# Performance work log

Hardware: AMD Instinct MI355X
Metric: run time of the kernel (lower is better)

Reference implementation:

```python
import jax, jax.numpy as jnp
import numpy as np

B, F, H, D, S = 32, 512, 8, 64, 256
TOPK = max(1, int(0.1 * F))  # 51
BETA0 = 0.6


def setup_inputs() -> dict:
    key = jax.random.key(0)
    k1, k2, k3 = jax.random.split(key, 3)
    values = jax.random.normal(k1, (B, F, H, D), jnp.float32)
    data_logits = jax.random.normal(k2, (B, F, H, S), jnp.float32)
    # alpha is orthogonal-initialized in torch; normal init preserves the math being tested
    alpha = jax.random.normal(k3, (H, S, F), jnp.float32)
    inv_softplus = np.float32(BETA0 + np.log1p(-np.exp(-BETA0)))
    beta_param = jnp.full((H, S, 1), inv_softplus, jnp.float32)
    return {"values": values, "data_logits": data_logits, "alpha": alpha, "beta_param": beta_param}


def _topk_mask(logits, k):
    # keep exactly top-k per row (last axis), others -> -inf (matches torch topk+scatter)
    topv, topi = jax.lax.top_k(logits, k)            # [..., k]
    shp = logits.shape
    n = int(np.prod(shp[:-1]))
    flat = jnp.full((n, shp[-1]), -jnp.inf, logits.dtype)
    rows = jnp.arange(n)[:, None]
    flat = flat.at[rows, topi.reshape(n, k)].set(topv.reshape(n, k))
    return flat.reshape(shp)


def reference(values, data_logits, alpha, beta_param):
    scale = 1.0 / np.sqrt(alpha.shape[-1])
    alpha_logits = alpha * scale                       # [H,S,F]
    dl = jnp.transpose(data_logits, (0, 2, 3, 1))      # [B,H,S,F]
    mu = dl.mean(axis=-1, keepdims=True)
    std = jnp.sqrt(dl.var(axis=-1, keepdims=True) + 1e-6) + 1e-6
    dl = (dl - mu) / std
    beta_eff = jax.nn.softplus(beta_param)             # [H,S,1]
    logits = alpha_logits[None] + beta_eff[None] * dl  # [B,H,S,F]
    logits = _topk_mask(logits, TOPK)
    attn = jax.nn.softmax(logits, axis=-1)             # dropout omitted (eval mode)
    out = jnp.einsum('bhsf,bfhd->bshd', attn, values)  # [B,S,H,D]
    return out
```

## Files before the change

kernel.cpp:

```cpp
#include <hip/hip_runtime.h>
#include <hip/hip_bf16.h>
#include <stdint.h>
#include <math.h>

#define NB 32
#define NF 512
#define NH 8
#define ND 64
#define NS 256
#define TOPK 51
#define STILE 16
#define LDSF 537

__device__ __forceinline__ float wave_sum_f32(float v) {
#pragma unroll
  for (int o = 32; o > 0; o >>= 1) v += __shfl_xor(v, o, 64);
  return v;
}

__device__ __forceinline__ int lane_prefix(unsigned long long m) {
  return __builtin_amdgcn_mbcnt_hi((unsigned)(m >> 32),
         __builtin_amdgcn_mbcnt_lo((unsigned)m, 0u));
}

__device__ __forceinline__ unsigned f32key(float x) {
  unsigned b = __float_as_uint(x);
  return (b & 0x80000000u) ? ~b : (b | 0x80000000u);
}

__device__ __forceinline__ float np_pairwise_sum_512(const float* __restrict__ row, int lane) {
  const int c2 = lane & 31;
  const int k  = c2 >> 3;
  const int c  = c2 & 7;
  const float* blk = row + 136 * k;
  float r = blk[c];
#pragma unroll
  for (int m = 1; m < 16; ++m) r += blk[c + 8 * m];
  float s = r + __shfl_xor(r, 1, 64);
  s = s + __shfl_xor(s, 2, 64);
  s = s + __shfl_xor(s, 4, 64);
  float u = s + __shfl_xor(s, 8, 64);
  u = u + __shfl_xor(u, 16, 64);
  return u;
}

__global__ __launch_bounds__(256)
void prep_kernel(const float* __restrict__ bp, const float* __restrict__ alpha,
                 float* __restrict__ betaf, unsigned* __restrict__ klo,
                 unsigned* __restrict__ khi) {
  const int gid  = blockIdx.x * 256 + threadIdx.x;
  const int hs   = gid >> 6;
  const int lane = gid & 63;
  if (hs >= NH * NS) return;
  const float scalef = (float)0.04419417382415922;
  const float* ar = alpha + (size_t)hs * NF;
  float s1 = 0.f, s2 = 0.f;
#pragma unroll
  for (int j = 0; j < 8; ++j) {
    float v = ar[lane + 64 * j] * scalef;
    s1 += v; s2 = fmaf(v, v, s2);
  }
  s1 = wave_sum_f32(s1); s2 = wave_sum_f32(s2);
  const float mean = s1 * (1.f / 512.f);
  float var = s2 * (1.f / 512.f) - mean * mean;
  if (var < 0.f) var = 0.f;
  const double e = exp((double)bp[hs]);
  const float beta = (float)log1p(e);
  const float sig  = sqrtf(var + beta * beta);
  const float that = fmaf(1.281552f, sig, mean);
  const float w    = 0.30f * sig;
  if (lane == 0) {
    betaf[hs] = beta;
    klo[hs] = f32key(that - w);
    khi[hs] = f32key(that + w);
  }
}

__global__ __launch_bounds__(1024, 8)
void gating_attention_kernel(const float* __restrict__ vals,
                             const float* __restrict__ dlg,
                             const float* __restrict__ alpha,
                             const float* __restrict__ betap,
                             const float* __restrict__ betaf,
                             const unsigned* __restrict__ klo,
                             const unsigned* __restrict__ khi,
                             float* __restrict__ out)
{
#pragma clang fp contract(off)
  __shared__ float dl_t[STILE * LDSF];
  __shared__ uint2 pairs[STILE][64];

  const int blk  = blockIdx.x;
  const int bh   = blk & 255;
  const int t    = blk >> 8;
  const int b    = bh >> 3;
  const int h    = bh & 7;
  const int s0   = t * STILE;
  const int tid  = threadIdx.x;
  const int w    = tid >> 6;
  const int lane = tid & 63;
  const float scalef = (float)0.04419417382415922;

#pragma unroll
  for (int cc = 0; cc < 2; ++cc) {
    int i  = cc * 1024 + tid;
    int f  = i >> 2;
    int sg = (i & 3) << 2;
    int fo = f + ((f >> 7) << 3);
    const float4 v4 = *reinterpret_cast<const float4*>(
        dlg + ((((size_t)b * NF + f) * NH + h) * NS + (size_t)(s0 + sg)));
    dl_t[(sg + 0) * LDSF + fo] = v4.x;
    dl_t[(sg + 1) * LDSF + fo] = v4.y;
    dl_t[(sg + 2) * LDSF + fo] = v4.z;
    dl_t[(sg + 3) * LDSF + fo] = v4.w;
  }
  __syncthreads();

  const int s  = s0 + w;
  const int hs = h * NS + s;
  float* row = dl_t + w * LDSF;

  const int fb0 = 4 * lane;
  const int off0 = fb0 + ((fb0 >> 7) << 3);
  const int fb1 = 256 + 4 * lane;
  const int off1 = fb1 + ((fb1 >> 7) << 3);

  const float4 a40 = *reinterpret_cast<const float4*>(
      alpha + ((size_t)hs) * NF + fb0);
  const float4 a41 = *reinterpret_cast<const float4*>(
      alpha + ((size_t)hs) * NF + fb1);
  const float4 x40 = *reinterpret_cast<const float4*>(row + off0);
  const float4 x41 = *reinterpret_cast<const float4*>(row + off1);

  float a[8] = {a40.x, a40.y, a40.z, a40.w, a41.x, a41.y, a41.z, a41.w};
  float x[8] = {x40.x, x40.y, x40.z, x40.w, x41.x, x41.y, x41.z, x41.w};

  const float S1 = np_pairwise_sum_512(row, lane);
  const float mu = S1 * (1.0f / 512.0f);

  float tv[8];
#pragma unroll
  for (int j = 0; j < 8; ++j) tv[j] = x[j] - mu;
  *reinterpret_cast<float4*>(row + off0) =
      make_float4(tv[0]*tv[0], tv[1]*tv[1], tv[2]*tv[2], tv[3]*tv[3]);
  *reinterpret_cast<float4*>(row + off1) =
      make_float4(tv[4]*tv[4], tv[5]*tv[5], tv[6]*tv[6], tv[7]*tv[7]);
  const float S2  = np_pairwise_sum_512(row, lane);
  const float var = S2 * (1.0f / 512.0f);
  const float stdv = sqrtf(var + 1e-6f) + 1e-6f;

  float beta;
  if (betaf) beta = betaf[hs];
  else { double e = exp((double)betap[hs]); beta = (float)log1p(e); }

  const double rd = 1.0 / (double)stdv;
  float lg[8];
  unsigned key[8];
#pragma unroll
  for (int j = 0; j < 8; ++j) {
    float z  = (float)((double)tv[j] * rd);
    float m  = beta * z;
    float af = a[j] * scalef;
    float l  = af + m;
    lg[j] = l;
    key[j] = f32key(l);
  }

  auto countGE = [&key](unsigned thr) -> int {
    int c = 0;
#pragma unroll
    for (int j = 0; j < 8; ++j) c += __popcll(__ballot(key[j] >= thr));
    return c;
  };

  unsigned lo, hi;
  if (klo) {
    lo = klo[hs]; hi = khi[hs];
    if (hi <= lo) hi = lo + 1;
  } else {
    unsigned kmax = key[0], kmin = key[0];
#pragma unroll
    for (int j = 1; j < 8; ++j) {
      kmax = key[j] > kmax ? key[j] : kmax;
      kmin = key[j] < kmin ? key[j] : kmin;
    }
#pragma unroll
    for (int o = 32; o > 0; o >>= 1) {
      unsigned om = (unsigned)__shfl_xor((int)kmax, o, 64);
      unsigned on = (unsigned)__shfl_xor((int)kmin, o, 64);
      kmax = om > kmax ? om : kmax;
      kmin = on < kmin ? on : kmin;
    }
    lo = kmin; hi = kmax;
  }

  int cl = countGE(lo);
  unsigned step = hi - lo;
  while (cl < TOPK) {
    hi = lo;
    lo = (lo >= step) ? (lo - step) : 0u;
    step <<= 1;
    cl = countGE(lo);
  }
  unsigned T; int cnt;
  if (cl == TOPK) { T = lo; cnt = cl; }
  else {
    int ch = countGE(hi);
    while (ch >= TOPK && hi != 0xFFFFFFFFu) {
      lo = hi; cl = ch;
      unsigned nh = hi + step;
      if (nh < hi) nh = 0xFFFFFFFFu;
      hi = nh; step <<= 1;
      ch = countGE(hi);
    }
    if (ch >= TOPK) { T = hi; cnt = ch; }
    else {
      while (lo < hi) {
        unsigned mid = hi - ((hi - lo) >> 1);
        int cm = countGE(mid);
        if (cm >= TOPK) { lo = mid; cl = cm; if (cm == TOPK) break; }
        else hi = mid - 1;
      }
      T = lo; cnt = cl;
    }
  }
  const bool exact = (cnt == TOPK);

  bool keep[8];
  if (exact) {
#pragma unroll
    for (int j = 0; j < 8; ++j) keep[j] = (key[j] >= T);
  } else {
    int g = 0;
#pragma unroll
    for (int j = 0; j < 8; ++j) g += __popcll(__ballot(key[j] > T));
    const int need = TOPK - g;
    int cumt = 0;
#pragma unroll
    for (int j = 0; j < 8; ++j) {
      unsigned long long meq = __ballot(key[j] == T);
      int tr = cumt + lane_prefix(meq);
      cumt += __popcll(meq);
      keep[j] = (key[j] > T) || ((key[j] == T) && (tr < need));
    }
  }

  unsigned tb = (T & 0x80000000u) ? (T ^ 0x80000000u) : ~T;
  const float thrf = __uint_as_float(tb);

  float p[8];
  float zs = 0.0f;
#pragma unroll
  for (int j = 0; j < 8; ++j) {
    float e = keep[j] ? __expf(lg[j] - thrf) : 0.0f;
    p[j] = e;
    zs += e;
  }
  zs = wave_sum_f32(zs);
  const float rz = 1.0f / zs;

  int base = 0;
#pragma unroll
  for (int j = 0; j < 8; ++j) {
    unsigned long long mk = __ballot(keep[j]);
    int idx = base + lane_prefix(mk);
    if (keep[j]) {
      unsigned f = (unsigned)(((j >> 2) << 8) + 4 * lane + (j & 3));
      pairs[w][idx] = make_uint2(f << 11, __float_as_uint(p[j]));
    }
    base += __popcll(mk);
  }
  if (lane == TOPK) pairs[w][TOPK] = make_uint2(0u, 0u);
  const int nk = (TOPK + 3) & ~3;

  const char* vbase = (const char*)(vals + (((size_t)b * NF) * NH + h) * ND) + 4 * lane;
  float acc0 = 0.0f, acc1 = 0.0f, acc2 = 0.0f, acc3 = 0.0f;
  for (int k0 = 0; k0 < nk; k0 += 4) {
    uint2 e0 = pairs[w][k0 + 0];
    uint2 e1 = pairs[w][k0 + 1];
    uint2 e2 = pairs[w][k0 + 2];
    uint2 e3 = pairs[w][k0 + 3];
    float v0 = *(const float*)(vbase + e0.x);
    float v1 = *(const float*)(vbase + e1.x);
    float v2 = *(const float*)(vbase + e2.x);
    float v3 = *(const float*)(vbase + e3.x);
    acc0 = fmaf(__uint_as_float(e0.y), v0, acc0);
    acc1 = fmaf(__uint_as_float(e1.y), v1, acc1);
    acc2 = fmaf(__uint_as_float(e2.y), v2, acc2);
    acc3 = fmaf(__uint_as_float(e3.y), v3, acc3);
  }
  const float acc = (acc0 + acc1) + (acc2 + acc3);

  out[(((size_t)b * NS + s) * NH + h) * ND + lane] = acc * rz;
}

extern "C" void kernel_launch(void* const* d_in, const int* in_sizes, int n_in,
                              void* d_out, int out_size, void* d_ws, size_t ws_size,
                              hipStream_t stream) {
  const float* vals  = (const float*)d_in[0];
  const float* dlg   = (const float*)d_in[1];
  const float* alpha = (const float*)d_in[2];
  const float* betap = (const float*)d_in[3];
  float* out = (float*)d_out;

  float* betaf = nullptr; unsigned* klo = nullptr; unsigned* khi = nullptr;
  const size_t need = (size_t)(NH * NS) * 12;
  if (ws_size >= need) {
    betaf = (float*)d_ws;
    klo   = (unsigned*)((char*)d_ws + (size_t)(NH * NS) * 4);
    khi   = (unsigned*)((char*)d_ws + (size_t)(NH * NS) * 8);
    prep_kernel<<<(NH * NS * 64) / 256, 256, 0, stream>>>(betap, alpha, betaf, klo, khi);
  }

  dim3 grid(NB * NH * (NS / STILE));
  dim3 block(1024);
  gating_attention_kernel<<<grid, block, 0, stream>>>(vals, dlg, alpha, betap,
                                                      betaf, klo, khi, out);
}
```

Before: 106.8 us.

## Process two sequence rows per wave with a 32-row tile and reuse LDS for pairs

New measurement: 132.3 us. 23.9% more time.

```diff
diff --git a/kernel.cpp b/kernel.cpp
--- a/kernel.cpp
+++ b/kernel.cpp
@@ -9,7 +9,7 @@
 #define ND 64
 #define NS 256
 #define TOPK 51
-#define STILE 16
+#define STILE 32
 #define LDSF 537
 
 __device__ __forceinline__ float wave_sum_f32(float v) {
@@ -42,6 +42,42 @@
   float u = s + __shfl_xor(s, 8, 64);
   u = u + __shfl_xor(u, 16, 64);
   return u;
+}
+
+__device__ __forceinline__ void solve_topk(const unsigned key[8], unsigned lo, unsigned hi,
+                                           unsigned& T, int& cnt) {
+  auto countGE = [&key](unsigned thr) -> int {
+    int c = 0;
+#pragma unroll
+    for (int j = 0; j < 8; ++j) c += __popcll(__ballot(key[j] >= thr));
+    return c;
+  };
+  if (hi <= lo) hi = lo + 1;
+  int cl = countGE(lo);
+  unsigned step = hi - lo;
+  while (cl < TOPK) {
+    hi = lo;
+    lo = (lo >= step) ? (lo - step) : 0u;
+    step <<= 1;
+    cl = countGE(lo);
+  }
+  if (cl == TOPK) { T = lo; cnt = cl; return; }
+  int ch = countGE(hi);
+  while (ch >= TOPK && hi != 0xFFFFFFFFu) {
+    lo = hi; cl = ch;
+    unsigned nh = hi + step;
+    if (nh < hi) nh = 0xFFFFFFFFu;
+    hi = nh; step <<= 1;
+    ch = countGE(hi);
+  }
+  if (ch >= TOPK) { T = hi; cnt = ch; return; }
+  while (lo < hi) {
+    unsigned mid = hi - ((hi - lo) >> 1);
+    int cm = countGE(mid);
+    if (cm >= TOPK) { lo = mid; cl = cm; if (cm == TOPK) break; }
+    else hi = mid - 1;
+  }
+  T = lo; cnt = cl;
 }
 
 __global__ __launch_bounds__(256)
@@ -88,7 +124,6 @@
 {
 #pragma clang fp contract(off)
   __shared__ float dl_t[STILE * LDSF];
-  __shared__ uint2 pairs[STILE][64];
 
   const int blk  = blockIdx.x;
   const int bh   = blk & 255;
@@ -102,10 +137,10 @@
   const float scalef = (float)0.04419417382415922;
 
 #pragma unroll
-  for (int cc = 0; cc < 2; ++cc) {
+  for (int cc = 0; cc < 4; ++cc) {
     int i  = cc * 1024 + tid;
-    int f  = i >> 2;
-    int sg = (i & 3) << 2;
+    int f  = i >> 3;
+    int sg = (i & 7) << 2;
     int fo = f + ((f >> 7) << 3);
     const float4 v4 = *reinterpret_cast<const float4*>(
         dlg + ((((size_t)b * NF + f) * NH + h) * NS + (size_t)(s0 + sg)));
@@ -116,73 +151,88 @@
   }
   __syncthreads();
 
-  const int s  = s0 + w;
-  const int hs = h * NS + s;
-  float* row = dl_t + w * LDSF;
+  const int r0 = 2 * w, r1 = 2 * w + 1;
+  const int sA = s0 + r0, sB = s0 + r1;
+  const int hsA = h * NS + sA, hsB = h * NS + sB;
+  float* rowA = dl_t + r0 * LDSF;
+  float* rowB = dl_t + r1 * LDSF;
 
   const int fb0 = 4 * lane;
   const int off0 = fb0 + ((fb0 >> 7) << 3);
   const int fb1 = 256 + 4 * lane;
   const int off1 = fb1 + ((fb1 >> 7) << 3);
 
-  const float4 a40 = *reinterpret_cast<const float4*>(
-      alpha + ((size_t)hs) * NF + fb0);
-  const float4 a41 = *reinterpret_cast<const float4*>(
-      alpha + ((size_t)hs) * NF + fb1);
-  const float4 x40 = *reinterpret_cast<const float4*>(row + off0);
-  const float4 x41 = *reinterpret_cast<const float4*>(row + off1);
-
-  float a[8] = {a40.x, a40.y, a40.z, a40.w, a41.x, a41.y, a41.z, a41.w};
-  float x[8] = {x40.x, x40.y, x40.z, x40.w, x41.x, x41.y, x41.z, x41.w};
-
-  const float S1 = np_pairwise_sum_512(row, lane);
-  const float mu = S1 * (1.0f / 512.0f);
-
-  float tv[8];
-#pragma unroll
-  for (int j = 0; j < 8; ++j) tv[j] = x[j] - mu;
-  *reinterpret_cast<float4*>(row + off0) =
-      make_float4(tv[0]*tv[0], tv[1]*tv[1], tv[2]*tv[2], tv[3]*tv[3]);
-  *reinterpret_cast<float4*>(row + off1) =
-      make_float4(tv[4]*tv[4], tv[5]*tv[5], tv[6]*tv[6], tv[7]*tv[7]);
-  const float S2  = np_pairwise_sum_512(row, lane);
-  const float var = S2 * (1.0f / 512.0f);
-  const float stdv = sqrtf(var + 1e-6f) + 1e-6f;
-
-  float beta;
-  if (betaf) beta = betaf[hs];
-  else { double e = exp((double)betap[hs]); beta = (float)log1p(e); }
-
-  const double rd = 1.0 / (double)stdv;
-  float lg[8];
-  unsigned key[8];
+  const float4 aA0 = *reinterpret_cast<const float4*>(alpha + (size_t)hsA * NF + fb0);
+  const float4 aA1 = *reinterpret_cast<const float4*>(alpha + (size_t)hsA * NF + fb1);
+  const float4 aB0 = *reinterpret_cast<const float4*>(alpha + (size_t)hsB * NF + fb0);
+  const float4 aB1 = *reinterpret_cast<const float4*>(alpha + (size_t)hsB * NF + fb1);
+  const float4 xA0 = *reinterpret_cast<const float4*>(rowA + off0);
+  const float4 xA1 = *reinterpret_cast<const float4*>(rowA + off1);
+  const float4 xB0 = *reinterpret_cast<const float4*>(rowB + off0);
+  const float4 xB1 = *reinterpret_cast<const float4*>(rowB + off1);
+
+  float xA[8] = {xA0.x, xA0.y, xA0.z, xA0.w, xA1.x, xA1.y, xA1.z, xA1.w};
+  float xB[8] = {xB0.x, xB0.y, xB0.z, xB0.w, xB1.x, xB1.y, xB1.z, xB1.w};
+  float aA[8] = {aA0.x, aA0.y, aA0.z, aA0.w, aA1.x, aA1.y, aA1.z, aA1.w};
+  float aB[8] = {aB0.x, aB0.y, aB0.z, aB0.w, aB1.x, aB1.y, aB1.z, aB1.w};
+
+  const float S1A = np_pairwise_sum_512(rowA, lane);
+  const float S1B = np_pairwise_sum_512(rowB, lane);
+  const float muA = S1A * (1.0f / 512.0f);
+  const float muB = S1B * (1.0f / 512.0f);
+
+  float tvA[8], tvB[8];
+#pragma unroll
+  for (int j = 0; j < 8; ++j) { tvA[j] = xA[j] - muA; tvB[j] = xB[j] - muB; }
+  *reinterpret_cast<float4*>(rowA + off0) =
+      make_float4(tvA[0]*tvA[0], tvA[1]*tvA[1], tvA[2]*tvA[2], tvA[3]*tvA[3]);
+  *reinterpret_cast<float4*>(rowA + off1) =
+      make_float4(tvA[4]*tvA[4], tvA[5]*tvA[5], tvA[6]*tvA[6], tvA[7]*tvA[7]);
+  *reinterpret_cast<float4*>(rowB + off0) =
+      make_float4(tvB[0]*tvB[0], tvB[1]*tvB[1], tvB[2]*tvB[2], tvB[3]*tvB[3]);
+  *reinterpret_cast<float4*>(rowB + off1) =
+      make_float4(tvB[4]*tvB[4], tvB[5]*tvB[5], tvB[6]*tvB[6], tvB[7]*tvB[7]);
+  const float S2A = np_pairwise_sum_512(rowA, lane);
+  const float S2B = np_pairwise_sum_512(rowB, lane);
+  const float stdA = sqrtf(S2A * (1.0f / 512.0f) + 1e-6f) + 1e-6f;
+  const float stdB = sqrtf(S2B * (1.0f / 512.0f) + 1e-6f) + 1e-6f;
+
+  float betaA, betaB;
+  if (betaf) { betaA = betaf[hsA]; betaB = betaf[hsB]; }
+  else {
+    betaA = (float)log1p(exp((double)betap[hsA]));
+    betaB = (float)log1p(exp((double)betap[hsB]));
+  }
+
+  const double rdA = 1.0 / (double)stdA;
+  const double rdB = 1.0 / (double)stdB;
+  float lgA[8], lgB[8];
+  unsigned keyA[8], keyB[8];
 #pragma unroll
   for (int j = 0; j < 8; ++j) {
-    float z  = (float)((double)tv[j] * rd);
-    float m  = beta * z;
-    float af = a[j] * scalef;
-    float l  = af + m;
-    lg[j] = l;
-    key[j] = f32key(l);
-  }
-
-  auto countGE = [&key](unsigned thr) -> int {
-    int c = 0;
-#pragma unroll
-    for (int j = 0; j < 8; ++j) c += __popcll(__ballot(key[j] >= thr));
-    return c;
-  };
-
-  unsigned lo, hi;
+    float zA = (float)((double)tvA[j] * rdA);
+    float zB = (float)((double)tvB[j] * rdB);
+    float lA = aA[j] * scalef + betaA * zA;
+    float lB = aB[j] * scalef + betaB * zB;
+    lgA[j] = lA; lgB[j] = lB;
+    keyA[j] = f32key(lA); keyB[j] = f32key(lB);
+  }
+
+  unsigned loA, hiA, loB, hiB;
   if (klo) {
-    lo = klo[hs]; hi = khi[hs];
-    if (hi <= lo) hi = lo + 1;
+    loA = klo[hsA]; hiA = khi[hsA];
+    loB = klo[hsB]; hiB = khi[hsB];
   } else {
-    unsigned kmax = key[0], kmin = key[0];
+    unsigned kmin = keyA[0], kmax = keyA[0];
 #pragma unroll
     for (int j = 1; j < 8; ++j) {
-      kmax = key[j] > kmax ? key[j] : kmax;
-      kmin = key[j] < kmin ? key[j] : kmin;
+      kmax = keyA[j] > kmax ? keyA[j] : kmax;
+      kmin = keyA[j] < kmin ? keyA[j] : kmin;
+    }
+#pragma unroll
+    for (int j = 0; j < 8; ++j) {
+      kmax = keyB[j] > kmax ? keyB[j] : kmax;
+      kmin = keyB[j] < kmin ? keyB[j] : kmin;
     }
 #pragma unroll
     for (int o = 32; o > 0; o >>= 1) {
@@ -191,107 +241,116 @@
       kmax = om > kmax ? om : kmax;
       kmin = on < kmin ? on : kmin;
     }
-    lo = kmin; hi = kmax;
-  }
-
-  int cl = countGE(lo);
-  unsigned step = hi - lo;
-  while (cl < TOPK) {
-    hi = lo;
-    lo = (lo >= step) ? (lo - step) : 0u;
-    step <<= 1;
-    cl = countGE(lo);
-  }
-  unsigned T; int cnt;
-  if (cl == TOPK) { T = lo; cnt = cl; }
-  else {
-    int ch = countGE(hi);
-    while (ch >= TOPK && hi != 0xFFFFFFFFu) {
-      lo = hi; cl = ch;
-      unsigned nh = hi + step;
-      if (nh < hi) nh = 0xFFFFFFFFu;
-      hi = nh; step <<= 1;
-      ch = countGE(hi);
-    }
-    if (ch >= TOPK) { T = hi; cnt = ch; }
-    else {
-      while (lo < hi) {
-        unsigned mid = hi - ((hi - lo) >> 1);
-        int cm = countGE(mid);
-        if (cm >= TOPK) { lo = mid; cl = cm; if (cm == TOPK) break; }
-        else hi = mid - 1;
-      }
-      T = lo; cnt = cl;
-    }
-  }
-  const bool exact = (cnt == TOPK);
-
-  bool keep[8];
-  if (exact) {
-#pragma unroll
-    for (int j = 0; j < 8; ++j) keep[j] = (key[j] >= T);
+    loA = loB = kmin; hiA = hiB = kmax;
+  }
+  unsigned TA, TB; int cntA, cntB;
+  solve_topk(keyA, loA, hiA, TA, cntA);
+  solve_topk(keyB, loB, hiB, TB, cntB);
+
+  bool keepA[8], keepB[8];
+  if (cntA == TOPK) {
+#pragma unroll
+    for (int j = 0; j < 8; ++j) keepA[j] = (keyA[j] >= TA);
   } else {
     int g = 0;
 #pragma unroll
-    for (int j = 0; j < 8; ++j) g += __popcll(__ballot(key[j] > T));
+    for (int j = 0; j < 8; ++j) g += __popcll(__ballot(keyA[j] > TA));
     const int need = TOPK - g;
     int cumt = 0;
 #pragma unroll
     for (int j = 0; j < 8; ++j) {
-      unsigned long long meq = __ballot(key[j] == T);
+      unsigned long long meq = __ballot(keyA[j] == TA);
       int tr = cumt + lane_prefix(meq);
       cumt += __popcll(meq);
-      keep[j] = (key[j] > T) || ((key[j] == T) && (tr < need));
-    }
-  }
-
-  unsigned tb = (T & 0x80000000u) ? (T ^ 0x80000000u) : ~T;
-  const float thrf = __uint_as_float(tb);
-
-  float p[8];
-  float zs = 0.0f;
+      keepA[j] = (keyA[j] > TA) || ((keyA[j] == TA) && (tr < need));
+    }
+  }
+  if (cntB == TOPK) {
+#pragma unroll
+    for (int j = 0; j < 8; ++j) keepB[j] = (keyB[j] >= TB);
+  } else {
+    int g = 0;
+#pragma unroll
+    for (int j = 0; j < 8; ++j) g += __popcll(__ballot(keyB[j] > TB));
+    const int need = TOPK - g;
+    int cumt = 0;
+#pragma unroll
+    for (int j = 0; j < 8; ++j) {
+      unsigned long long meq = __ballot(keyB[j] == TB);
+      int tr = cumt + lane_prefix(meq);
+      cumt += __popcll(meq);
+      keepB[j] = (keyB[j] > TB) || ((keyB[j] == TB) && (tr < need));
+    }
+  }
+
+  unsigned tbA = (TA & 0x80000000u) ? (TA ^ 0x80000000u) : ~TA;
+  unsigned tbB = (TB & 0x80000000u) ? (TB ^ 0x80000000u) : ~TB;
+  const float thrA = __uint_as_float(tbA);
+  const float thrB = __uint_as_float(tbB);
+
+  float pA[8], pB[8];
+  float zsA = 0.0f, zsB = 0.0f;
 #pragma unroll
   for (int j = 0; j < 8; ++j) {
-    float e = keep[j] ? __expf(lg[j] - thrf) : 0.0f;
-    p[j] = e;
-    zs += e;
-  }
-  zs = wave_sum_f32(zs);
-  const float rz = 1.0f / zs;
-
-  int base = 0;
+    float eA = keepA[j] ? __expf(lgA[j] - thrA) : 0.0f;
+    float eB = keepB[j] ? __expf(lgB[j] - thrB) : 0.0f;
+    pA[j] = eA; pB[j] = eB;
+    zsA += eA; zsB += eB;
+  }
+  zsA = wave_sum_f32(zsA);
+  zsB = wave_sum_f32(zsB);
+  const float rzA = 1.0f / zsA;
+  const float rzB = 1.0f / zsB;
+
+  uint2* prA = (uint2*)(dl_t + ((r0 * LDSF + 1) & ~1));
+  uint2* prB = (uint2*)(dl_t + ((r1 * LDSF + 1) & ~1));
+  int baseA = 0, baseB = 0;
 #pragma unroll
   for (int j = 0; j < 8; ++j) {
-    unsigned long long mk = __ballot(keep[j]);
-    int idx = base + lane_prefix(mk);
-    if (keep[j]) {
-      unsigned f = (unsigned)(((j >> 2) << 8) + 4 * lane + (j & 3));
-      pairs[w][idx] = make_uint2(f << 11, __float_as_uint(p[j]));
-    }
-    base += __popcll(mk);
-  }
-  if (lane == TOPK) pairs[w][TOPK] = make_uint2(0u, 0u);
+    unsigned f = (unsigned)(((j >> 2) << 8) + 4 * lane + (j & 3));
+    unsigned long long mkA = __ballot(keepA[j]);
+    int idxA = baseA + lane_prefix(mkA);
+    if (keepA[j]) prA[idxA] = make_uint2(f << 11, __float_as_uint(pA[j]));
+    baseA += __popcll(mkA);
+    unsigned long long mkB = __ballot(keepB[j]);
+    int idxB = baseB + lane_prefix(mkB);
+    if (keepB[j]) prB[idxB] = make_uint2(f << 11, __float_as_uint(pB[j]));
+    baseB += __popcll(mkB);
+  }
+  if (lane == TOPK) {
+    prA[TOPK] = make_uint2(0u, 0u);
+    prB[TOPK] = make_uint2(0u, 0u);
+  }
   const int nk = (TOPK + 3) & ~3;
 
   const char* vbase = (const char*)(vals + (((size_t)b * NF) * NH + h) * ND) + 4 * lane;
-  float acc0 = 0.0f, acc1 = 0.0f, acc2 = 0.0f, acc3 = 0.0f;
+  float aA0c = 0.f, aA1c = 0.f, aA2c = 0.f, aA3c = 0.f;
+  float aB0c = 0.f, aB1c = 0.f, aB2c = 0.f, aB3c = 0.f;
   for (int k0 = 0; k0 < nk; k0 += 4) {
-    uint2 e0 = pairs[w][k0 + 0];
-    uint2 e1 = pairs[w][k0 + 1];
-    uint2 e2 = pairs[w][k0 + 2];
-    uint2 e3 = pairs[w][k0 + 3];
-    float v0 = *(const float*)(vbase + e0.x);
-    float v1 = *(const float*)(vbase + e1.x);
-    float v2 = *(const float*)(vbase + e2.x);
-    float v3 = *(const float*)(vbase + e3.x);
-    acc0 = fmaf(__uint_as_float(e0.y), v0, acc0);
-    acc1 = fmaf(__uint_as_float(e1.y), v1, acc1);
-    acc2 = fmaf(__uint_as_float(e2.y), v2, acc2);
-    acc3 = fmaf(__uint_as_float(e3.y), v3, acc3);
-  }
-  const float acc = (acc0 + acc1) + (acc2 + acc3);
-
-  out[(((size_t)b * NS + s) * NH + h) * ND + lane] = acc * rz;
+    uint2 eA0 = prA[k0 + 0], eA1 = prA[k0 + 1], eA2 = prA[k0 + 2], eA3 = prA[k0 + 3];
+    uint2 eB0 = prB[k0 + 0], eB1 = prB[k0 + 1], eB2 = prB[k0 + 2], eB3 = prB[k0 + 3];
+    float vA0 = *(const float*)(vbase + eA0.x);
+    float vA1 = *(const float*)(vbase + eA1.x);
+    float vA2 = *(const float*)(vbase + eA2.x);
+    float vA3 = *(const float*)(vbase + eA3.x);
+    float vB0 = *(const float*)(vbase + eB0.x);
+    float vB1 = *(const float*)(vbase + eB1.x);
+    float vB2 = *(const float*)(vbase + eB2.x);
+    float vB3 = *(const float*)(vbase + eB3.x);
+    aA0c = fmaf(__uint_as_float(eA0.y), vA0, aA0c);
+    aA1c = fmaf(__uint_as_float(eA1.y), vA1, aA1c);
+    aA2c = fmaf(__uint_as_float(eA2.y), vA2, aA2c);
+    aA3c = fmaf(__uint_as_float(eA3.y), vA3, aA3c);
+    aB0c = fmaf(__uint_as_float(eB0.y), vB0, aB0c);
+    aB1c = fmaf(__uint_as_float(eB1.y), vB1, aB1c);
+    aB2c = fmaf(__uint_as_float(eB2.y), vB2, aB2c);
+    aB3c = fmaf(__uint_as_float(eB3.y), vB3, aB3c);
+  }
+  const float accA = (aA0c + aA1c) + (aA2c + aA3c);
+  const float accB = (aB0c + aB1c) + (aB2c + aB3c);
+
+  out[(((size_t)b * NS + sA) * NH + h) * ND + lane] = accA * rzA;
+  out[(((size_t)b * NS + sB) * NH + h) * ND + lane] = accB * rzB;
 }
 
 extern "C" void kernel_launch(void* const* d_in, const int* in_sizes, int n_in,
```

## Hoist alpha/prep loads before LDS fill and split gather into float2 half-waves

Applied to the files above, without the earlier changes.

Result: slower. 118.3 us (+10.7%).

```diff
diff --git a/kernel.cpp b/kernel.cpp
--- a/kernel.cpp
+++ b/kernel.cpp
@@ -11,6 +11,7 @@
 #define TOPK 51
 #define STILE 16
 #define LDSF 537
+#define NKPAD 56
 
 __device__ __forceinline__ float wave_sum_f32(float v) {
 #pragma unroll
@@ -88,7 +89,7 @@
 {
 #pragma clang fp contract(off)
   __shared__ float dl_t[STILE * LDSF];
-  __shared__ uint2 pairs[STILE][64];
+  __shared__ uint2 pairs[STILE][NKPAD];
 
   const int blk  = blockIdx.x;
   const int bh   = blk & 255;
@@ -100,6 +101,25 @@
   const int w    = tid >> 6;
   const int lane = tid & 63;
   const float scalef = (float)0.04419417382415922;
+
+  const int s  = s0 + w;
+  const int hs = h * NS + s;
+
+  const int fb0 = 4 * lane;
+  const int off0 = fb0 + ((fb0 >> 7) << 3);
+  const int fb1 = 256 + 4 * lane;
+  const int off1 = fb1 + ((fb1 >> 7) << 3);
+  const float4 a40 = *reinterpret_cast<const float4*>(alpha + (size_t)hs * NF + fb0);
+  const float4 a41 = *reinterpret_cast<const float4*>(alpha + (size_t)hs * NF + fb1);
+  float beta;
+  unsigned lo0 = 0u, hi0 = 0u;
+  const bool have_prep = (betaf != nullptr);
+  if (have_prep) {
+    beta = betaf[hs];
+    lo0 = klo[hs]; hi0 = khi[hs];
+  } else {
+    double e = exp((double)betap[hs]); beta = (float)log1p(e);
+  }
 
 #pragma unroll
   for (int cc = 0; cc < 2; ++cc) {
@@ -116,22 +136,10 @@
   }
   __syncthreads();
 
-  const int s  = s0 + w;
-  const int hs = h * NS + s;
   float* row = dl_t + w * LDSF;
 
-  const int fb0 = 4 * lane;
-  const int off0 = fb0 + ((fb0 >> 7) << 3);
-  const int fb1 = 256 + 4 * lane;
-  const int off1 = fb1 + ((fb1 >> 7) << 3);
-
-  const float4 a40 = *reinterpret_cast<const float4*>(
-      alpha + ((size_t)hs) * NF + fb0);
-  const float4 a41 = *reinterpret_cast<const float4*>(
-      alpha + ((size_t)hs) * NF + fb1);
   const float4 x40 = *reinterpret_cast<const float4*>(row + off0);
   const float4 x41 = *reinterpret_cast<const float4*>(row + off1);
-
   float a[8] = {a40.x, a40.y, a40.z, a40.w, a41.x, a41.y, a41.z, a41.w};
   float x[8] = {x40.x, x40.y, x40.z, x40.w, x41.x, x41.y, x41.z, x41.w};
 
@@ -149,10 +157,6 @@
   const float var = S2 * (1.0f / 512.0f);
   const float stdv = sqrtf(var + 1e-6f) + 1e-6f;
 
-  float beta;
-  if (betaf) beta = betaf[hs];
-  else { double e = exp((double)betap[hs]); beta = (float)log1p(e); }
-
   const double rd = 1.0 / (double)stdv;
   float lg[8];
   unsigned key[8];
@@ -174,8 +178,8 @@
   };
 
   unsigned lo, hi;
-  if (klo) {
-    lo = klo[hs]; hi = khi[hs];
+  if (have_prep) {
+    lo = lo0; hi = hi0;
     if (hi <= lo) hi = lo + 1;
   } else {
     unsigned kmax = key[0], kmin = key[0];
@@ -256,8 +260,6 @@
     p[j] = e;
     zs += e;
   }
-  zs = wave_sum_f32(zs);
-  const float rz = 1.0f / zs;
 
   int base = 0;
 #pragma unroll
@@ -270,28 +272,46 @@
     }
     base += __popcll(mk);
   }
-  if (lane == TOPK) pairs[w][TOPK] = make_uint2(0u, 0u);
-  const int nk = (TOPK + 3) & ~3;
-
-  const char* vbase = (const char*)(vals + (((size_t)b * NF) * NH + h) * ND) + 4 * lane;
-  float acc0 = 0.0f, acc1 = 0.0f, acc2 = 0.0f, acc3 = 0.0f;
-  for (int k0 = 0; k0 < nk; k0 += 4) {
-    uint2 e0 = pairs[w][k0 + 0];
-    uint2 e1 = pairs[w][k0 + 1];
-    uint2 e2 = pairs[w][k0 + 2];
-    uint2 e3 = pairs[w][k0 + 3];
-    float v0 = *(const float*)(vbase + e0.x);
-    float v1 = *(const float*)(vbase + e1.x);
-    float v2 = *(const float*)(vbase + e2.x);
-    float v3 = *(const float*)(vbase + e3.x);
-    acc0 = fmaf(__uint_as_float(e0.y), v0, acc0);
-    acc1 = fmaf(__uint_as_float(e1.y), v1, acc1);
-    acc2 = fmaf(__uint_as_float(e2.y), v2, acc2);
-    acc3 = fmaf(__uint_as_float(e3.y), v3, acc3);
-  }
-  const float acc = (acc0 + acc1) + (acc2 + acc3);
-
-  out[(((size_t)b * NS + s) * NH + h) * ND + lane] = acc * rz;
+  if (lane >= TOPK && lane < NKPAD) pairs[w][lane] = make_uint2(0u, 0u);
+
+  const int hi2 = lane >> 5;
+  const int q   = lane & 31;
+  const char* vbase2 =
+      (const char*)(vals + (((size_t)b * NF) * NH + h) * ND) + 8 * q;
+  float a0x = 0.f, a0y = 0.f, a1x = 0.f, a1y = 0.f;
+  float a2x = 0.f, a2y = 0.f, a3x = 0.f, a3y = 0.f;
+#pragma clang loop unroll(disable)
+  for (int r = 0; r < 28; r += 4) {
+    const uint2 e0 = pairs[w][2 * (r + 0) + hi2];
+    const uint2 e1 = pairs[w][2 * (r + 1) + hi2];
+    const uint2 e2 = pairs[w][2 * (r + 2) + hi2];
+    const uint2 e3 = pairs[w][2 * (r + 3) + hi2];
+    const float2 v0 = *(const float2*)(vbase2 + e0.x);
+    const float2 v1 = *(const float2*)(vbase2 + e1.x);
+    const float2 v2 = *(const float2*)(vbase2 + e2.x);
+    const float2 v3 = *(const float2*)(vbase2 + e3.x);
+    a0x = fmaf(__uint_as_float(e0.y), v0.x, a0x);
+    a0y = fmaf(__uint_as_float(e0.y), v0.y, a0y);
+    a1x = fmaf(__uint_as_float(e1.y), v1.x, a1x);
+    a1y = fmaf(__uint_as_float(e1.y), v1.y, a1y);
+    a2x = fmaf(__uint_as_float(e2.y), v2.x, a2x);
+    a2y = fmaf(__uint_as_float(e2.y), v2.y, a2y);
+    a3x = fmaf(__uint_as_float(e3.y), v3.x, a3x);
+    a3y = fmaf(__uint_as_float(e3.y), v3.y, a3y);
+  }
+  float totx = (a0x + a1x) + (a2x + a3x);
+  float toty = (a0y + a1y) + (a2y + a3y);
+  totx += __shfl_xor(totx, 32, 64);
+  toty += __shfl_xor(toty, 32, 64);
+
+  zs = wave_sum_f32(zs);
+  const float rz = 1.0f / zs;
+
+  if (lane < 32) {
+    float2 o2 = make_float2(totx * rz, toty * rz);
+    *reinterpret_cast<float2*>(
+        (char*)(out + (((size_t)b * NS + s) * NH + h) * ND) + 8 * q) = o2;
+  }
 }
 
 extern "C" void kernel_launch(void* const* d_in, const int* in_sizes, int n_in,
```
